# Kernel tuning notes

Measured on AMD Instinct MI355X. Metric: run time of the kernel, lower is better.

## Reference

```python
import jax, jax.numpy as jnp
import numpy as np

B, L, D_IN, D_EXP, N_EXP = 4, 2048, 1024, 1024, 8


def setup_inputs() -> dict:
    key = jax.random.key(0)
    ks = jax.random.split(key, 5)
    s_in = 1.0 / np.sqrt(D_IN)
    x = jax.random.normal(ks[0], (B, L, D_IN), dtype=jnp.float32)
    # per-expert Dense kernels/biases: (n, d_in, d_exp), (n, d_exp)
    We = jax.random.normal(ks[1], (N_EXP, D_IN, D_EXP), dtype=jnp.float32) * s_in
    be = jnp.zeros((N_EXP, D_EXP), dtype=jnp.float32)
    # gating Dense: (d_in, n), (n)
    Wg = jax.random.normal(ks[2], (D_IN, N_EXP), dtype=jnp.float32) * s_in
    bg = jnp.zeros((N_EXP,), dtype=jnp.float32)
    return {"x": x, "We": We, "be": be, "Wg": Wg, "bg": bg}


def reference(x, We, be, Wg, bg):
    # expert outputs: (b, l, n, d_exp) = relu(x @ We[n] + be[n])
    h = jax.nn.relu(jnp.einsum('bld,ndk->blnk', x, We) + be[None, None, :, :])
    # gate: softmax over experts, (b, l, n)
    gate = jax.nn.softmax(jnp.einsum('bld,dn->bln', x, Wg) + bg, axis=-1)
    # gated weighted sum over experts -> (b, l, d_exp)
    return jnp.einsum('bln,blnk->blk', gate, h)
```

## Files before the change

### kernel.cpp

```cpp
#include <hip/hip_runtime.h>
#include <hip/hip_bf16.h>
#include <stdint.h>

#define M_TOT 8192
#define DIN   1024
#define DEXP  1024
#define NEXP  8

#define BM 128
#define BN 256
#define BK 64
#define NT 128
#define TPE 16
#define SLOT_E 24576
#define EXPSZ (DEXP * DIN)

typedef __attribute__((ext_vector_type(8))) short bf16x8;
typedef __attribute__((ext_vector_type(4))) float f32x4;
typedef __attribute__((ext_vector_type(8))) unsigned short us8;

typedef __attribute__((address_space(1))) void* as1vp;
typedef __attribute__((address_space(3))) void* as3vp;

__device__ __forceinline__ unsigned short f2bf(float f) {
    union { float f; unsigned u; } v; v.f = f;
    return (unsigned short)((v.u + 0x7fffu + ((v.u >> 16) & 1u)) >> 16);
}

__device__ __forceinline__ void gl_lds16(const unsigned short* g, unsigned short* l) {
    __builtin_amdgcn_global_load_lds((as1vp)g, (as3vp)l, 16, 0, 0);
}

#define MFMA(va, vb, vc) __builtin_amdgcn_mfma_f32_16x16x32_bf16(va, vb, vc, 0, 0, 0)

__global__ __launch_bounds__(256) void cvt_x_k(const float* __restrict__ in,
                                               unsigned short* __restrict__ out, int n8) {
    int i = blockIdx.x * 256 + threadIdx.x;
    int stride = gridDim.x * 256;
    for (; i < n8; i += stride) {
        const float4* p = (const float4*)in + (size_t)i * 2;
        float4 a = p[0], b = p[1];
        us8 o;
        o[0] = f2bf(a.x); o[1] = f2bf(a.y); o[2] = f2bf(a.z); o[3] = f2bf(a.w);
        o[4] = f2bf(b.x); o[5] = f2bf(b.y); o[6] = f2bf(b.z); o[7] = f2bf(b.w);
        *(us8*)(out + (size_t)i * 8) = o;
    }
}

__global__ __launch_bounds__(256) void cvt_w_k(const float* __restrict__ We,
                                               unsigned short* __restrict__ Wt) {
    __shared__ float tile[64][65];
    int n  = blockIdx.z;
    int k0 = blockIdx.y * 64;
    int j0 = blockIdx.x * 64;
    int t  = threadIdx.x;
    int tr = t >> 6, tc = t & 63;
    const float* src = We + (size_t)n * DIN * DEXP;
    #pragma unroll
    for (int rr = 0; rr < 16; ++rr) {
        int r = rr * 4 + tr;
        tile[r][tc] = src[(size_t)(k0 + r) * DEXP + j0 + tc];
    }
    __syncthreads();
    unsigned short* dst = Wt + (size_t)n * DEXP * DIN;
    #pragma unroll
    for (int rr = 0; rr < 16; ++rr) {
        int r = rr * 4 + tr;
        dst[(size_t)(j0 + r) * DIN + k0 + tc] = f2bf(tile[tc][r]);
    }
}

__global__ __launch_bounds__(256) void gate_k(const float* __restrict__ x,
                                              const float* __restrict__ Wg,
                                              const float* __restrict__ bg,
                                              float* __restrict__ gate) {
    __shared__ float wgt[NEXP][DIN];
    int t = threadIdx.x;
    for (int idx = t; idx < DIN * NEXP; idx += 256)
        wgt[idx & 7][idx >> 3] = Wg[idx];
    __syncthreads();
    int wid = t >> 6, lane = t & 63;
    for (int m = blockIdx.x * 4 + wid; m < M_TOT; m += gridDim.x * 4) {
        const float* xr = x + (size_t)m * DIN;
        float acc[NEXP];
        #pragma unroll
        for (int n = 0; n < NEXP; ++n) acc[n] = 0.f;
        for (int i = 0; i < DIN / 64; ++i) {
            int d = i * 64 + lane;
            float xv = xr[d];
            #pragma unroll
            for (int n = 0; n < NEXP; ++n) acc[n] = fmaf(xv, wgt[n][d], acc[n]);
        }
        #pragma unroll
        for (int n = 0; n < NEXP; ++n) {
            #pragma unroll
            for (int off = 32; off; off >>= 1) acc[n] += __shfl_xor(acc[n], off);
            acc[n] += bg[n];
        }
        float mx = acc[0];
        #pragma unroll
        for (int n = 1; n < NEXP; ++n) mx = fmaxf(mx, acc[n]);
        float s = 0.f, e[NEXP];
        #pragma unroll
        for (int n = 0; n < NEXP; ++n) { e[n] = __expf(acc[n] - mx); s += e[n]; }
        float inv = 1.f / s;
        if (lane < NEXP) gate[(size_t)m * NEXP + lane] = e[lane] * inv;
    }
}

__global__ __launch_bounds__(512, 2) void moe_k(const unsigned short* __restrict__ Xb,
                                                const unsigned short* __restrict__ Wt,
                                                const float* __restrict__ gate,
                                                const float* __restrict__ be,
                                                float* __restrict__ out) {
    __shared__ __align__(16) unsigned short lds[3 * SLOT_E];
    __shared__ float gateL[BM * NEXP];
    __shared__ float biasL[NEXP * BN];

    const int t    = threadIdx.x;
    const int lane = t & 63;
    const int wv   = t >> 6;
    const int wm   = wv >> 2;
    const int wn   = wv & 3;
    const int l16  = lane & 15;
    const int lk   = lane >> 4;

    const int b    = blockIdx.x;
    const int lg   = (b & 7) * 32 + (b >> 3);
    const int brow = (lg >> 2) * BM;
    const int bcol = (lg & 3) * BN;

    const int r1     = t >> 3;
    const int srcOff = r1 * DIN + (((t & 7) ^ (r1 & 7)) * 8);
    const unsigned short* gA = Xb + (size_t)brow * DIN;
    const unsigned short* gB = Wt + (size_t)bcol * DIN;

    const int xr    = (l16 & 7) * 8;
    const int kc0   = (lk * 8) ^ xr;
    const int kc1   = (32 + lk * 8) ^ xr;
    const int aBase = (wm * 64 + l16) * 64;
    const int bBase = 8192 + (wn * 64 + l16) * 64;

#define STAGE_A(sl_, k0_) do { \
    const unsigned short* g_ = gA + (k0_) + srcOff; \
    unsigned short* d_ = (unsigned short*)lds + (sl_) * SLOT_E + t * 8; \
    gl_lds16(g_, d_); gl_lds16(g_ + 64 * DIN, d_ + 4096); } while (0)
#define STAGE_B0(sl_, e_, k0_) do { \
    const unsigned short* g_ = gB + (size_t)(e_) * EXPSZ + (k0_) + srcOff; \
    unsigned short* d_ = (unsigned short*)lds + (sl_) * SLOT_E + 8192 + t * 8; \
    gl_lds16(g_, d_); gl_lds16(g_ + 64 * DIN, d_ + 4096); } while (0)
#define STAGE_B1(sl_, e_, k0_) do { \
    const unsigned short* g_ = gB + (size_t)(e_) * EXPSZ + 128 * DIN + (k0_) + srcOff; \
    unsigned short* d_ = (unsigned short*)lds + (sl_) * SLOT_E + 16384 + t * 8; \
    gl_lds16(g_, d_); gl_lds16(g_ + 64 * DIN, d_ + 4096); } while (0)

    f32x4 acc_e[4][4] = {};
    f32x4 acc_o[4][4] = {};

    {
        const float* gp = gate + (size_t)brow * NEXP;
        gateL[t]       = gp[t];
        gateL[t + 512] = gp[t + 512];
        #pragma unroll
        for (int i = 0; i < 4; ++i) {
            int idx = t + i * 512;
            biasL[idx] = be[(size_t)(idx >> 8) * DEXP + bcol + (idx & 255)];
        }
    }
    STAGE_A(0, 0);  STAGE_B0(0, 0, 0);  STAGE_B1(0, 0, 0);
    STAGE_A(1, 64); STAGE_B0(1, 0, 64); STAGE_B1(1, 0, 64);
    asm volatile("s_waitcnt vmcnt(6)" ::: "memory");
    asm volatile("s_waitcnt lgkmcnt(0)" ::: "memory");
    __builtin_amdgcn_s_barrier();

    int sl = 0, sl2 = 2;
    for (int T = 0; T < NT; ++T) {
        const unsigned short* L = lds + sl * SLOT_E;
        const int e2 = (T + 2) >> 4;
        const int k2 = ((T + 2) & (TPE - 1)) * BK;
        const bool doSt = (T < NT - 2);

        bf16x8 a0[4], b0[4], a1[4], b1[4];

        #pragma unroll
        for (int mi = 0; mi < 4; ++mi) a0[mi] = *(const bf16x8*)(L + aBase + mi * 1024 + kc0);
        #pragma unroll
        for (int ni = 0; ni < 4; ++ni) b0[ni] = *(const bf16x8*)(L + bBase + ni * 1024 + kc0);
        if (doSt) { STAGE_A(sl2, k2); STAGE_B0(sl2, e2, k2); }
        __builtin_amdgcn_s_barrier();
        asm volatile("s_waitcnt lgkmcnt(0)" ::: "memory");
        __builtin_amdgcn_sched_barrier(0);
        __builtin_amdgcn_s_setprio(1);
        #pragma unroll
        for (int mi = 0; mi < 4; ++mi)
            #pragma unroll
            for (int ni = 0; ni < 4; ++ni)
                acc_e[mi][ni] = MFMA(a0[mi], b0[ni], acc_e[mi][ni]);
        __builtin_amdgcn_s_setprio(0);
        __builtin_amdgcn_s_barrier();

        #pragma unroll
        for (int mi = 0; mi < 4; ++mi) a1[mi] = *(const bf16x8*)(L + aBase + mi * 1024 + kc1);
        #pragma unroll
        for (int ni = 0; ni < 4; ++ni) b1[ni] = *(const bf16x8*)(L + bBase + ni * 1024 + kc1);
        if (doSt) {
            STAGE_B1(sl2, e2, k2);
            asm volatile("s_waitcnt vmcnt(6)" ::: "memory");
        } else {
            asm volatile("s_waitcnt vmcnt(0)" ::: "memory");
        }
        __builtin_amdgcn_s_barrier();
        asm volatile("s_waitcnt lgkmcnt(0)" ::: "memory");
        __builtin_amdgcn_sched_barrier(0);
        __builtin_amdgcn_s_setprio(1);
        #pragma unroll
        for (int mi = 0; mi < 4; ++mi)
            #pragma unroll
            for (int ni = 0; ni < 4; ++ni)
                acc_e[mi][ni] = MFMA(a1[mi], b1[ni], acc_e[mi][ni]);
        __builtin_amdgcn_s_setprio(0);
        __builtin_amdgcn_s_barrier();

        if ((T & (TPE - 1)) == (TPE - 1)) {
            const int e = T >> 4;
            float bias[4];
            #pragma unroll
            for (int ni = 0; ni < 4; ++ni)
                bias[ni] = biasL[e * BN + wn * 64 + ni * 16 + l16];
            #pragma unroll
            for (int mi = 0; mi < 4; ++mi) {
                #pragma unroll
                for (int r = 0; r < 4; ++r) {
                    const int rl = wm * 64 + mi * 16 + lk * 4 + r;
                    const float g = gateL[rl * NEXP + e];
                    #pragma unroll
                    for (int ni = 0; ni < 4; ++ni)
                        acc_o[mi][ni][r] += g * fmaxf(acc_e[mi][ni][r] + bias[ni], 0.f);
                }
            }
            #pragma unroll
            for (int mi = 0; mi < 4; ++mi)
                #pragma unroll
                for (int ni = 0; ni < 4; ++ni)
                    acc_e[mi][ni] = (f32x4){0.f, 0.f, 0.f, 0.f};
        }

        sl  = (sl  == 2) ? 0 : sl  + 1;
        sl2 = (sl2 == 2) ? 0 : sl2 + 1;
    }

    #pragma unroll
    for (int mi = 0; mi < 4; ++mi) {
        #pragma unroll
        for (int r = 0; r < 4; ++r) {
            const int row = brow + wm * 64 + mi * 16 + lk * 4 + r;
            float* op = out + (size_t)row * DEXP + bcol + wn * 64 + l16;
            #pragma unroll
            for (int ni = 0; ni < 4; ++ni) op[ni * 16] = acc_o[mi][ni][r];
        }
    }
#undef STAGE_A
#undef STAGE_B0
#undef STAGE_B1
}

extern "C" void kernel_launch(void* const* d_in, const int* in_sizes, int n_in,
                              void* d_out, int out_size, void* d_ws, size_t ws_size,
                              hipStream_t stream) {
    const float* x  = (const float*)d_in[0];
    const float* We = (const float*)d_in[1];
    const float* be = (const float*)d_in[2];
    const float* Wg = (const float*)d_in[3];
    const float* bg = (const float*)d_in[4];
    float* out = (float*)d_out;

    unsigned short* Xb = (unsigned short*)d_ws;
    unsigned short* Wt = Xb + (size_t)M_TOT * DIN;
    float* gate = (float*)(Wt + (size_t)NEXP * DEXP * DIN);

    hipLaunchKernelGGL(cvt_x_k, dim3(2048), dim3(256), 0, stream, x, Xb, M_TOT * DIN / 8);
    hipLaunchKernelGGL(cvt_w_k, dim3(16, 16, 8), dim3(256), 0, stream, We, Wt);
    hipLaunchKernelGGL(gate_k, dim3(512), dim3(256), 0, stream, x, Wg, bg, gate);
    hipLaunchKernelGGL(moe_k, dim3((M_TOT / BM) * (DEXP / BN)), dim3(512), 0, stream,
                       Xb, Wt, gate, be, out);
}
```

Measured before the change: 168.7 us.

## Process two experts per k-step with 256x128 tiles sharing A fragments

Reshapes the block tile from 128x256 with BK=64 to 256x128 with BK=32. Each k-step now computes two experts at once, with separate accumulators, and both reuse the same A fragment loaded from LDS. This cuts LDS reads of A and changes the global load mix toward more reuse of X per byte of weights. It also adds a second 64-register accumulator set, which raises register pressure under launch_bounds(512,2), and halves K per step, which doubles the barriers per unit of work.

```diff
diff --git a/kernel.cpp b/kernel.cpp
--- a/kernel.cpp
+++ b/kernel.cpp
@@ -7,12 +7,12 @@
 #define DEXP  1024
 #define NEXP  8
 
-#define BM 128
-#define BN 256
-#define BK 64
+#define BM 256
+#define BN 128
+#define BK 32
 #define NT 128
-#define TPE 16
-#define SLOT_E 24576
+#define KPP 32
+#define SLOT_E 16384
 #define EXPSZ (DEXP * DIN)
 
 typedef __attribute__((ext_vector_type(8))) short bf16x8;
@@ -120,73 +120,66 @@
     const int t    = threadIdx.x;
     const int lane = t & 63;
     const int wv   = t >> 6;
-    const int wm   = wv >> 2;
-    const int wn   = wv & 3;
+    const int wm   = wv >> 1;
+    const int wn   = wv & 1;
     const int l16  = lane & 15;
     const int lk   = lane >> 4;
 
     const int b    = blockIdx.x;
     const int lg   = (b & 7) * 32 + (b >> 3);
-    const int brow = (lg >> 2) * BM;
-    const int bcol = (lg & 3) * BN;
-
-    const int r1     = t >> 3;
-    const int srcOff = r1 * DIN + (((t & 7) ^ (r1 & 7)) * 8);
+    const int brow = (lg >> 3) * BM;
+    const int bcol = (lg & 7) * BN;
+
+    const int sA = (t >> 2) * DIN + ((((t & 3) ^ ((t >> 2) & 3))) * 8);
     const unsigned short* gA = Xb + (size_t)brow * DIN;
     const unsigned short* gB = Wt + (size_t)bcol * DIN;
 
-    const int xr    = (l16 & 7) * 8;
-    const int kc0   = (lk * 8) ^ xr;
-    const int kc1   = (32 + lk * 8) ^ xr;
-    const int aBase = (wm * 64 + l16) * 64;
-    const int bBase = 8192 + (wn * 64 + l16) * 64;
+    const int xc    = ((lk ^ (l16 & 3)) * 8);
+    const int aOff  = (wm * 64 + l16) * 32 + xc;
+    const int bOff  = 8192 + (wn * 64 + l16) * 32 + xc;
 
 #define STAGE_A(sl_, k0_) do { \
-    const unsigned short* g_ = gA + (k0_) + srcOff; \
+    const unsigned short* g_ = gA + (k0_) + sA; \
     unsigned short* d_ = (unsigned short*)lds + (sl_) * SLOT_E + t * 8; \
-    gl_lds16(g_, d_); gl_lds16(g_ + 64 * DIN, d_ + 4096); } while (0)
+    gl_lds16(g_, d_); gl_lds16(g_ + 128 * DIN, d_ + 4096); } while (0)
 #define STAGE_B0(sl_, e_, k0_) do { \
-    const unsigned short* g_ = gB + (size_t)(e_) * EXPSZ + (k0_) + srcOff; \
-    unsigned short* d_ = (unsigned short*)lds + (sl_) * SLOT_E + 8192 + t * 8; \
-    gl_lds16(g_, d_); gl_lds16(g_ + 64 * DIN, d_ + 4096); } while (0)
+    gl_lds16(gB + (size_t)(e_) * EXPSZ + (k0_) + sA, \
+             (unsigned short*)lds + (sl_) * SLOT_E + 8192 + t * 8); } while (0)
 #define STAGE_B1(sl_, e_, k0_) do { \
-    const unsigned short* g_ = gB + (size_t)(e_) * EXPSZ + 128 * DIN + (k0_) + srcOff; \
-    unsigned short* d_ = (unsigned short*)lds + (sl_) * SLOT_E + 16384 + t * 8; \
-    gl_lds16(g_, d_); gl_lds16(g_ + 64 * DIN, d_ + 4096); } while (0)
-
-    f32x4 acc_e[4][4] = {};
-    f32x4 acc_o[4][4] = {};
+    gl_lds16(gB + (size_t)(e_) * EXPSZ + (k0_) + sA, \
+             (unsigned short*)lds + (sl_) * SLOT_E + 12288 + t * 8); } while (0)
+
+    f32x4 acc_e0[4][4] = {};
+    f32x4 acc_e1[4][4] = {};
+    f32x4 acc_o[4][4]  = {};
 
     {
         const float* gp = gate + (size_t)brow * NEXP;
-        gateL[t]       = gp[t];
-        gateL[t + 512] = gp[t + 512];
-        #pragma unroll
-        for (int i = 0; i < 4; ++i) {
-            int idx = t + i * 512;
-            biasL[idx] = be[(size_t)(idx >> 8) * DEXP + bcol + (idx & 255)];
-        }
-    }
-    STAGE_A(0, 0);  STAGE_B0(0, 0, 0);  STAGE_B1(0, 0, 0);
-    STAGE_A(1, 64); STAGE_B0(1, 0, 64); STAGE_B1(1, 0, 64);
-    asm volatile("s_waitcnt vmcnt(6)" ::: "memory");
+        ((float4*)gateL)[t] = ((const float4*)gp)[t];
+        if (t < 256)
+            ((float4*)biasL)[t] =
+                *(const float4*)(be + (size_t)(t >> 5) * DEXP + bcol + (t & 31) * 4);
+    }
+    STAGE_A(0, 0);  STAGE_B0(0, 0, 0);  STAGE_B1(0, 1, 0);
+    STAGE_A(1, 32); STAGE_B0(1, 0, 32); STAGE_B1(1, 1, 32);
+    asm volatile("s_waitcnt vmcnt(4)" ::: "memory");
     asm volatile("s_waitcnt lgkmcnt(0)" ::: "memory");
     __builtin_amdgcn_s_barrier();
 
     int sl = 0, sl2 = 2;
     for (int T = 0; T < NT; ++T) {
         const unsigned short* L = lds + sl * SLOT_E;
-        const int e2 = (T + 2) >> 4;
-        const int k2 = ((T + 2) & (TPE - 1)) * BK;
+        const int p2  = (T + 2) >> 5;
+        const int k2  = ((T + 2) & (KPP - 1)) * BK;
         const bool doSt = (T < NT - 2);
 
-        bf16x8 a0[4], b0[4], a1[4], b1[4];
-
-        #pragma unroll
-        for (int mi = 0; mi < 4; ++mi) a0[mi] = *(const bf16x8*)(L + aBase + mi * 1024 + kc0);
-        #pragma unroll
-        for (int ni = 0; ni < 4; ++ni) b0[ni] = *(const bf16x8*)(L + bBase + ni * 1024 + kc0);
-        if (doSt) { STAGE_A(sl2, k2); STAGE_B0(sl2, e2, k2); }
+        bf16x8 a[4], b0[4], b1[4];
+
+        #pragma unroll
+        for (int mi = 0; mi < 4; ++mi) a[mi]  = *(const bf16x8*)(L + aOff + mi * 512);
+        #pragma unroll
+        for (int ni = 0; ni < 4; ++ni) b0[ni] = *(const bf16x8*)(L + bOff + ni * 512);
+        if (doSt) STAGE_A(sl2, k2);
         __builtin_amdgcn_s_barrier();
         asm volatile("s_waitcnt lgkmcnt(0)" ::: "memory");
         __builtin_amdgcn_sched_barrier(0);
@@ -195,17 +188,16 @@
         for (int mi = 0; mi < 4; ++mi)
             #pragma unroll
             for (int ni = 0; ni < 4; ++ni)
-                acc_e[mi][ni] = MFMA(a0[mi], b0[ni], acc_e[mi][ni]);
+                acc_e0[mi][ni] = MFMA(a[mi], b0[ni], acc_e0[mi][ni]);
         __builtin_amdgcn_s_setprio(0);
         __builtin_amdgcn_s_barrier();
 
         #pragma unroll
-        for (int mi = 0; mi < 4; ++mi) a1[mi] = *(const bf16x8*)(L + aBase + mi * 1024 + kc1);
-        #pragma unroll
-        for (int ni = 0; ni < 4; ++ni) b1[ni] = *(const bf16x8*)(L + bBase + ni * 1024 + kc1);
+        for (int ni = 0; ni < 4; ++ni) b1[ni] = *(const bf16x8*)(L + bOff + 4096 + ni * 512);
         if (doSt) {
-            STAGE_B1(sl2, e2, k2);
-            asm volatile("s_waitcnt vmcnt(6)" ::: "memory");
+            STAGE_B0(sl2, p2 * 2, k2);
+            STAGE_B1(sl2, p2 * 2 + 1, k2);
+            asm volatile("s_waitcnt vmcnt(4)" ::: "memory");
         } else {
             asm volatile("s_waitcnt vmcnt(0)" ::: "memory");
         }
@@ -217,32 +209,39 @@
         for (int mi = 0; mi < 4; ++mi)
             #pragma unroll
             for (int ni = 0; ni < 4; ++ni)
-                acc_e[mi][ni] = MFMA(a1[mi], b1[ni], acc_e[mi][ni]);
+                acc_e1[mi][ni] = MFMA(a[mi], b1[ni], acc_e1[mi][ni]);
         __builtin_amdgcn_s_setprio(0);
         __builtin_amdgcn_s_barrier();
 
-        if ((T & (TPE - 1)) == (TPE - 1)) {
-            const int e = T >> 4;
-            float bias[4];
-            #pragma unroll
-            for (int ni = 0; ni < 4; ++ni)
-                bias[ni] = biasL[e * BN + wn * 64 + ni * 16 + l16];
+        if ((T & (KPP - 1)) == (KPP - 1)) {
+            const int e0 = (T >> 5) * 2, e1 = e0 + 1;
+            float bi0[4], bi1[4];
+            #pragma unroll
+            for (int ni = 0; ni < 4; ++ni) {
+                bi0[ni] = biasL[e0 * BN + wn * 64 + ni * 16 + l16];
+                bi1[ni] = biasL[e1 * BN + wn * 64 + ni * 16 + l16];
+            }
             #pragma unroll
             for (int mi = 0; mi < 4; ++mi) {
                 #pragma unroll
                 for (int r = 0; r < 4; ++r) {
                     const int rl = wm * 64 + mi * 16 + lk * 4 + r;
-                    const float g = gateL[rl * NEXP + e];
+                    const float g0 = gateL[rl * NEXP + e0];
+                    const float g1 = gateL[rl * NEXP + e1];
                     #pragma unroll
-                    for (int ni = 0; ni < 4; ++ni)
-                        acc_o[mi][ni][r] += g * fmaxf(acc_e[mi][ni][r] + bias[ni], 0.f);
+                    for (int ni = 0; ni < 4; ++ni) {
+                        acc_o[mi][ni][r] += g0 * fmaxf(acc_e0[mi][ni][r] + bi0[ni], 0.f)
+                                          + g1 * fmaxf(acc_e1[mi][ni][r] + bi1[ni], 0.f);
+                    }
                 }
             }
             #pragma unroll
             for (int mi = 0; mi < 4; ++mi)
                 #pragma unroll
-                for (int ni = 0; ni < 4; ++ni)
-                    acc_e[mi][ni] = (f32x4){0.f, 0.f, 0.f, 0.f};
+                for (int ni = 0; ni < 4; ++ni) {
+                    acc_e0[mi][ni] = (f32x4){0.f, 0.f, 0.f, 0.f};
+                    acc_e1[mi][ni] = (f32x4){0.f, 0.f, 0.f, 0.f};
+                }
         }
 
         sl  = (sl  == 2) ? 0 : sl  + 1;
```

New measurement: 163.9 us. -2.9%, faster.
